# Performance work log

Measured on AMD Instinct MI355X. Metric: run time of the kernel, lower is better.

## Reference

```python
import math
import jax, jax.numpy as jnp
import numpy as np

L, B, D = 2048, 8, 1024
Z, H, N = 128, 2048, 16


def setup_inputs() -> dict:
    key = jax.random.key(0)
    ks = jax.random.split(key, 16)
    s = 0.02
    inp = {
        "x": jax.random.normal(ks[0], (L, B, D), jnp.float32),
        "ln_w": jnp.ones((D,), jnp.float32),
        "ln_b": jnp.zeros((D,), jnp.float32),
        "v_w": jax.random.normal(ks[1], (H, D), jnp.float32) * s,
        "v_b": jnp.zeros((H,), jnp.float32),
        "mx_w": jax.random.normal(ks[2], (Z + H + 2 * D, D), jnp.float32) * s,
        "mx_b": jnp.zeros((Z + H + 2 * D,), jnp.float32),
        "h_w": jax.random.normal(ks[3], (D, H), jnp.float32) * s,
        "h_b": jnp.zeros((D,), jnp.float32),
        "qk_gamma": jnp.ones((2, Z), jnp.float32) + jax.random.normal(ks[4], (2, Z), jnp.float32) * s,
        "qk_beta": jax.random.normal(ks[5], (2, Z), jnp.float32) * s,
        "ema_delta": jax.random.normal(ks[6], (D, N, 1), jnp.float32),
        "ema_alpha": jax.random.normal(ks[7], (D, N, 1), jnp.float32),
        "ema_beta": jax.random.normal(ks[8], (D, N, 1), jnp.float32) * s,
        "ema_gamma": jax.random.normal(ks[9], (D, N), jnp.float32) * s,
        "ema_omega": jax.random.normal(ks[10], (D,), jnp.float32) * s,
        "rb_alpha": jax.random.normal(ks[11], (1, Z), jnp.float32) * s,
        "rb_beta": jax.random.normal(ks[12], (1, Z), jnp.float32) * s,
    }
    return inp


def _rotary_bias(rb_alpha, rb_beta, seq_len, z):
    # RotaryRelativePositionalBias.forward(seq_len) -> (L, L)
    half = z // 2
    freqs = jnp.exp(jnp.arange(half, dtype=jnp.float32) * (-math.log(10000.0) / half))
    pos = jnp.arange(seq_len, dtype=jnp.float32)[:, None] * freqs[None, :]  # (L, half)
    sin, cos = jnp.sin(pos), jnp.cos(pos)

    def rot(w):  # (1, Z) -> (L, Z)
        we = jnp.broadcast_to(w, (seq_len, z))
        w1, w2 = we[:, :half], we[:, half:]
        return jnp.concatenate([w1 * cos - w2 * sin, w2 * cos + w1 * sin], axis=1)

    return rot(rb_alpha) @ rot(rb_beta).T  # (L, L)


def _ema(xn, ema_delta, ema_alpha, ema_beta, ema_gamma, ema_omega):
    # xn: (L, B, D) -> damped multi-head EMA via FFT causal conv (MEGA MultiHeadEMA)
    seq_len = xn.shape[0]
    p = jax.nn.sigmoid(ema_delta)           # (D, N, 1)
    a = jax.nn.sigmoid(ema_alpha)           # (D, N, 1)
    q = 1.0 - p * a                         # (D, N, 1)
    t = jnp.arange(seq_len, dtype=jnp.float32)[None, None, :]
    kern = (p * ema_beta) * jnp.exp(t * jnp.log(q))          # (D, N, L)
    scale = math.sqrt(1.0 / kern.shape[1])
    k_dl = jnp.einsum("dnl,dn->dl", kern, ema_gamma * scale)  # (D, L)
    xt = jnp.transpose(xn, (1, 2, 0))        # (B, D, L)
    nfft = 2 * seq_len
    kf = jnp.fft.rfft(k_dl, n=nfft)          # (D, F)
    xf = jnp.fft.rfft(xt, n=nfft)            # (B, D, F)
    conv = jnp.fft.irfft(xf * kf, n=nfft)[..., :seq_len]      # (B, D, L)
    return jax.nn.silu(jnp.transpose(conv, (2, 0, 1)) + xn * ema_omega)  # (L, B, D)


def reference(x, ln_w, ln_b, v_w, v_b, mx_w, mx_b, h_w, h_b, qk_gamma, qk_beta,
              ema_delta, ema_alpha, ema_beta, ema_gamma, ema_omega, rb_alpha, rb_beta):
    seq_len, bsz, d = x.shape
    residual = x
    # prenorm LayerNorm
    mu = jnp.mean(x, axis=-1, keepdims=True)
    var = jnp.mean(jnp.square(x - mu), axis=-1, keepdims=True)
    xn = (x - mu) * jax.lax.rsqrt(var + 1e-5) * ln_w + ln_b

    v = jax.nn.silu(xn @ v_w.T + v_b)                          # (L, B, H)
    mx = _ema(xn, ema_delta, ema_alpha, ema_beta, ema_gamma, ema_omega)
    base = mx @ mx_w.T + mx_b                                  # (L, B, Z+H+2D)
    u = jax.nn.sigmoid(base[..., :d])                          # update gate
    zr = jax.nn.silu(base[..., d:d + Z + H])
    hx = base[..., d + Z + H:]
    z, r = zr[..., :Z], zr[..., Z:]                            # (L,B,Z), (L,B,H)
    z2 = z[:, :, None, :] * qk_gamma + qk_beta                 # (L, B, 2, Z)
    q = jnp.transpose(z2[:, :, 0], (1, 0, 2)) * (Z ** -0.5)    # (B, L, Z)
    k = jnp.transpose(z2[:, :, 1], (1, 0, 2))                  # (B, L, Z)
    vb = jnp.transpose(v, (1, 0, 2))                           # (B, L, H)

    bias = _rotary_bias(rb_alpha, rb_beta, seq_len, Z)         # (L, L)
    attn = jax.nn.softmax(jnp.einsum("blz,bmz->blm", q, k) + bias, axis=-1)
    h = jnp.transpose(jnp.einsum("blm,bmh->blh", attn, vb), (1, 0, 2))  # (L, B, H)
    h = jax.nn.silu(hx + (h * r) @ h_w.T + h_b)                # (L, B, D)
    return residual + u * (h - residual)
```

## Files before the change

kernel.cpp:

```cpp
#include <hip/hip_runtime.h>
#include <cstdint>
#include <cstddef>

typedef __bf16 bf16;
typedef __bf16 bf16x8 __attribute__((ext_vector_type(8)));
typedef float  f32x4  __attribute__((ext_vector_type(4)));

#define DEVI static __device__ __forceinline__

DEVI float fsigmoid(float x) { return 1.0f / (1.0f + __expf(-x)); }
DEVI float fsilu(float x)    { return x / (1.0f + __expf(-x)); }

DEVI unsigned short b16bits(float v) { bf16 h = (bf16)v; return __builtin_bit_cast(unsigned short, h); }
DEVI float lo16f(unsigned int w) { return __builtin_bit_cast(float, w << 16); }
DEVI float hi16f(unsigned int w) { return __builtin_bit_cast(float, w & 0xffff0000u); }

DEVI float waveRedSum(float v) {
#pragma unroll
  for (int o = 32; o > 0; o >>= 1) v += __shfl_xor(v, o, 64);
  return v;
}
DEVI float waveRedMax(float v) {
#pragma unroll
  for (int o = 32; o > 0; o >>= 1) v = fmaxf(v, __shfl_xor(v, o, 64));
  return v;
}

DEVI void xcd_swizzle(int& bx, int& by) {
  const int gx = gridDim.x, gy = gridDim.y;
  const int nwg = gx * gy;
  const int flat = blockIdx.y * gx + blockIdx.x;
  const int xcd = flat & 7;
  const int rem = nwg & 7;
  const int q = nwg >> 3;
  const int base = (xcd < rem) ? xcd * (q + 1) : rem * (q + 1) + (xcd - rem) * q;
  const int swz = base + (flat >> 3);
  bx = swz % gx;
  by = swz / gx;
}

struct alignas(8) B4 { bf16 x, y, z, w; };

__global__ __launch_bounds__(256) void k_copyout(const float* __restrict__ x, float* __restrict__ o)
{
  const long i = (long)blockIdx.x * 256 + threadIdx.x;
  ((float4*)o)[i] = ((const float4*)x)[i];
}

__global__ __launch_bounds__(256) void k_lnstats(const float* __restrict__ x, float* __restrict__ stats)
{
  const long t = blockIdx.x;
  const int tid = threadIdx.x;
  const float4 v = ((const float4*)(x + t * 1024))[tid];
  float s  = v.x + v.y + v.z + v.w;
  float s2 = v.x * v.x + v.y * v.y + v.z * v.z + v.w * v.w;
  __shared__ float red[2][4];
  s = waveRedSum(s);
  s2 = waveRedSum(s2);
  const int wv = tid >> 6, ln = tid & 63;
  if (ln == 0) { red[0][wv] = s; red[1][wv] = s2; }
  __syncthreads();
  if (tid == 0) {
    s  = red[0][0] + red[0][1] + red[0][2] + red[0][3];
    s2 = red[1][0] + red[1][1] + red[1][2] + red[1][3];
    const float mu  = s * (1.0f / 1024.0f);
    const float var = s2 * (1.0f / 1024.0f) - mu * mu;
    stats[2 * t]     = mu;
    stats[2 * t + 1] = rsqrtf(var + 1e-5f);
  }
}

__global__ __launch_bounds__(256) void k_cvt(const float* __restrict__ in, bf16* __restrict__ out, int n4)
{
  const int i = blockIdx.x * 256 + threadIdx.x;
  if (i >= n4) return;
  const float4 v = ((const float4*)in)[i];
  B4 h; h.x = (bf16)v.x; h.y = (bf16)v.y; h.z = (bf16)v.z; h.w = (bf16)v.w;
  ((B4*)out)[i] = h;
}

__global__ __launch_bounds__(256) void k_ema_coeff(
    const float* __restrict__ de, const float* __restrict__ al,
    const float* __restrict__ be, const float* __restrict__ ga,
    float* __restrict__ qv, float* __restrict__ cv)
{
  const int i = blockIdx.x * 256 + threadIdx.x;
  const int d = i >> 4, n = i & 15;
  const float p = 1.0f / (1.0f + expf(-de[i]));
  const float a = 1.0f / (1.0f + expf(-al[i]));
  qv[n * 1024 + d] = 1.0f - p * a;
  cv[n * 1024 + d] = p * be[i] * ga[i] * 0.25f;
}

__global__ __launch_bounds__(256) void k_ema(
    const float* __restrict__ x, const float* __restrict__ stats,
    const float* __restrict__ lnw, const float* __restrict__ lnb,
    const float* __restrict__ qv, const float* __restrict__ cv,
    const float* __restrict__ omega, bf16* __restrict__ mx)
{
  const int d = blockIdx.x * 256 + threadIdx.x;
  const int b = blockIdx.y;
  float q[16], c[16], s[16];
#pragma unroll
  for (int n = 0; n < 16; ++n) {
    q[n] = qv[n * 1024 + d];
    c[n] = cv[n * 1024 + d];
    s[n] = 0.0f;
  }
  const float om = omega[d], wd = lnw[d], bd = lnb[d];
  const float* xp = x + (long)b * 1024 + d;
  bf16* mp = mx + (long)b * 1024 + d;
  float buf[8], nxt[8];
  float2 bst[8], nst[8];
#pragma unroll
  for (int i = 0; i < 8; ++i) {
    buf[i] = xp[(long)i * 8192];
    bst[i] = ((const float2*)stats)[(long)i * 8 + b];
  }
  for (int l0 = 0; l0 < 2048; l0 += 8) {
    if (l0 + 8 < 2048) {
#pragma unroll
      for (int i = 0; i < 8; ++i) {
        nxt[i] = xp[(long)(l0 + 8 + i) * 8192];
        nst[i] = ((const float2*)stats)[(long)(l0 + 8 + i) * 8 + b];
      }
    }
#pragma unroll
    for (int i = 0; i < 8; ++i) {
      const float xv = (buf[i] - bst[i].x) * bst[i].y * wd + bd;
      float p0 = 0.f, p1 = 0.f, p2 = 0.f, p3 = 0.f;
#pragma unroll
      for (int n = 0; n < 16; n += 4) {
        s[n]     = fmaf(q[n],     s[n],     xv);
        s[n + 1] = fmaf(q[n + 1], s[n + 1], xv);
        s[n + 2] = fmaf(q[n + 2], s[n + 2], xv);
        s[n + 3] = fmaf(q[n + 3], s[n + 3], xv);
        p0 = fmaf(c[n],     s[n],     p0);
        p1 = fmaf(c[n + 1], s[n + 1], p1);
        p2 = fmaf(c[n + 2], s[n + 2], p2);
        p3 = fmaf(c[n + 3], s[n + 3], p3);
      }
      const float pre = fmaf(xv, om, (p0 + p1) + (p2 + p3));
      mp[(long)(l0 + i) * 8192] = (bf16)fsilu(pre);
    }
#pragma unroll
    for (int i = 0; i < 8; ++i) { buf[i] = nxt[i]; bst[i] = nst[i]; }
  }
}

__global__ __launch_bounds__(64) void k_rotfill(
    const float* __restrict__ rba, const float* __restrict__ rbb,
    bf16* __restrict__ Qp, bf16* __restrict__ Kp)
{
  const int l = blockIdx.x, zi = threadIdx.x;
  const float fr = __expf(-0.14391156831212787f * (float)zi);
  const float pos = (float)l * fr;
  const float sn = sinf(pos), cs = cosf(pos);
  const float a1 = rba[zi], a2 = rba[64 + zi];
  const float b1 = rbb[zi], b2 = rbb[64 + zi];
  const bf16 qa = (bf16)(a1 * cs - a2 * sn);
  const bf16 qb = (bf16)(a2 * cs + a1 * sn);
  const bf16 ka = (bf16)(b1 * cs - b2 * sn);
  const bf16 kb = (bf16)(b2 * cs + b1 * sn);
#pragma unroll
  for (int b = 0; b < 8; ++b) {
    const long base = ((long)b * 2048 + l) * 256;
    Qp[base + 128 + zi] = qa;
    Qp[base + 192 + zi] = qb;
    Kp[base + 128 + zi] = ka;
    Kp[base + 192 + zi] = kb;
  }
}

__global__ __launch_bounds__(256) void k_softmax(float* __restrict__ S)
{
  const long row = blockIdx.x;
  float* sp = S + row * 2048;
  const int tid = threadIdx.x;
  float vals[8];
  float mx = -1e30f;
#pragma unroll
  for (int i = 0; i < 8; ++i) { vals[i] = sp[i * 256 + tid]; mx = fmaxf(mx, vals[i]); }
  __shared__ float red[4];
  mx = waveRedMax(mx);
  const int wv = tid >> 6, ln = tid & 63;
  if (ln == 0) red[wv] = mx;
  __syncthreads();
  mx = fmaxf(fmaxf(red[0], red[1]), fmaxf(red[2], red[3]));
  float sum = 0.f;
#pragma unroll
  for (int i = 0; i < 8; ++i) { vals[i] = __expf(vals[i] - mx); sum += vals[i]; }
  __syncthreads();
  sum = waveRedSum(sum);
  if (ln == 0) red[wv] = sum;
  __syncthreads();
  sum = red[0] + red[1] + red[2] + red[3];
  const float inv = 1.0f / sum;
  bf16* pp = (bf16*)sp;
#pragma unroll
  for (int i = 0; i < 8; ++i) pp[i * 256 + tid] = (bf16)(vals[i] * inv);
}

__global__ __launch_bounds__(1024) void k_vtrans8(
    const bf16* __restrict__ v, bf16* __restrict__ vt, const int eoff)
{
  __shared__ bf16 tile[32][33];
  const int l0 = blockIdx.x * 32, h0 = blockIdx.y * 32, b = blockIdx.z;
  const int tx = threadIdx.x, ty = threadIdx.y;
  tile[ty][tx] = v[((long)(l0 + ty) * 8 + b) * 256 + h0 + tx];
  __syncthreads();
  vt[((long)b * 2048 + eoff + h0 + ty) * 2048 + l0 + tx] = tile[tx][ty];
}

DEVI void gload16(const void* g, void* l) {
  __builtin_amdgcn_global_load_lds(
      (__attribute__((address_space(1))) void*)(void*)g,
      (__attribute__((address_space(3))) void*)l, 16, 0, 0);
}

template<int EPI>
__global__ __launch_bounds__(256) void k_gemm_bt(
    const bf16* __restrict__ A, const bf16* __restrict__ Bm,
    const int K, const int lda, const int ldb,
    const float* __restrict__ bias,
    void* __restrict__ o0, void* __restrict__ o1, void* __restrict__ o2, void* __restrict__ o3,
    const void* __restrict__ e0, const void* __restrict__ e1, const void* __restrict__ e2)
{
  __shared__ alignas(16) bf16 As[128 * 64];
  __shared__ alignas(16) bf16 Bs[128 * 64];
  const int tid = threadIdx.x;
  const int wave = tid >> 6, lane = tid & 63;
  const int wm = wave >> 1, wn = wave & 1;
  int bx, by;
  xcd_swizzle(bx, by);
  const int tm = by * 128, tn = bx * 128;
  const int fr = lane & 15, kg = lane >> 4;

  f32x4 acc[4][4];
  const f32x4 z4 = {0.0f, 0.0f, 0.0f, 0.0f};
#pragma unroll
  for (int i = 0; i < 4; ++i)
#pragma unroll
    for (int j = 0; j < 4; ++j) acc[i][j] = z4;

  const int est = wave * 512 + lane * 8;
  const int srow = est >> 6;
  const int scol = est & 63;
  const long arow = (long)(tm + srow);
  const long brow = (long)(tn + srow);

  for (int k0 = 0; k0 < K; k0 += 64) {
    __syncthreads();
#pragma unroll
    for (int cc = 0; cc < 4; ++cc) {
      gload16(A + (arow + cc * 32) * lda + k0 + scol, As + cc * 2048 + wave * 512);
      gload16(Bm + (brow + cc * 32) * ldb + k0 + scol, Bs + cc * 2048 + wave * 512);
    }
    __syncthreads();
    bf16x8 af[2][4], bfv[2][4];
#pragma unroll
    for (int ks = 0; ks < 2; ++ks)
#pragma unroll
      for (int i = 0; i < 4; ++i) {
        af[ks][i]  = *(const bf16x8*)&As[(wm * 64 + i * 16 + fr) * 64 + ks * 32 + kg * 8];
        bfv[ks][i] = *(const bf16x8*)&Bs[(wn * 64 + i * 16 + fr) * 64 + ks * 32 + kg * 8];
      }
#pragma unroll
    for (int ks = 0; ks < 2; ++ks)
#pragma unroll
      for (int i = 0; i < 4; ++i)
#pragma unroll
        for (int j = 0; j < 4; ++j)
          acc[i][j] = __builtin_amdgcn_mfma_f32_16x16x32_bf16(af[ks][i], bfv[ks][j], acc[i][j], 0, 0, 0);
  }

#pragma unroll
  for (int i = 0; i < 4; ++i) {
#pragma unroll
    for (int j = 0; j < 4; ++j) {
#pragma unroll
      for (int rr = 0; rr < 4; ++rr) {
        const int row = tm + wm * 64 + i * 16 + kg * 4 + rr;
        const int col = tn + wn * 64 + j * 16 + fr;
        const float a = acc[i][j][rr];
        if constexpr (EPI == 1) {
          const float tv = a + bias[col];
          if (col < 1024) {
            ((unsigned short*)o0)[((long)row * 1024 + col) * 2] = b16bits(fsigmoid(tv));
          } else if (col < 1152) {
            const int zi = col - 1024;
            const float zval = fsilu(tv);
            const float qq = (zval * ((const float*)e0)[zi] + ((const float*)e1)[zi]) * 0.08838834764831845f;
            const float kk =  zval * ((const float*)e0)[128 + zi] + ((const float*)e1)[128 + zi];
            const long base = ((long)(row & 7) * 2048 + (row >> 3)) * 256 + zi;
            ((bf16*)o2)[base] = (bf16)qq;
            ((bf16*)o3)[base] = (bf16)kk;
          } else if (col < 3200) {
            ((bf16*)o1)[(long)row * 2048 + (col - 1152)] = (bf16)fsilu(tv);
          } else {
            ((unsigned short*)o0)[((long)row * 1024 + (col - 3200)) * 2 + 1] = b16bits(tv);
          }
        } else if constexpr (EPI == 2) {
          ((float*)o0)[(long)row * 2048 + col] = a;
        } else if constexpr (EPI == 3) {
          const long idx = (long)row * 16384 + col;
          const float rv = (float)((const bf16*)e0)[idx];
          ((bf16*)o0)[idx] = (bf16)(a * rv);
        } else if constexpr (EPI == 4) {
          const long idx = (long)row * 1024 + col;
          const unsigned int w = ((const unsigned int*)o0)[idx];
          const float uv = lo16f(w), hxv = hi16f(w);
          const float hval = fsilu(hxv + a + bias[col]);
          const float xv = ((const float*)e1)[idx];
          ((float*)o0)[idx] = xv + uv * (hval - xv);
        }
      }
    }
  }
}

__global__ __launch_bounds__(256) void k_gemm_lnA(
    const float* __restrict__ x, const float* __restrict__ stats,
    const float* __restrict__ lnw, const float* __restrict__ lnb,
    const bf16* __restrict__ Bm, const float* __restrict__ bias,
    bf16* __restrict__ out)
{
  __shared__ alignas(16) bf16 As[128 * 64];
  __shared__ alignas(16) bf16 Bs[128 * 64];
  __shared__ float smu[128], srs[128];
  const int tid = threadIdx.x;
  const int wave = tid >> 6, lane = tid & 63;
  const int wm = wave >> 1, wn = wave & 1;
  int bx, by;
  xcd_swizzle(bx, by);
  const int tm = by * 128, tn = bx * 128;
  const int fr = lane & 15, kg = lane >> 4;
  if (tid < 128) {
    smu[tid] = stats[2 * (long)(tm + tid)];
    srs[tid] = stats[2 * (long)(tm + tid) + 1];
  }

  f32x4 acc[4][4];
  const f32x4 z4 = {0.0f, 0.0f, 0.0f, 0.0f};
#pragma unroll
  for (int i = 0; i < 4; ++i)
#pragma unroll
    for (int j = 0; j < 4; ++j) acc[i][j] = z4;

  const int est = wave * 512 + lane * 8;
  const int srow = est >> 6, scol = est & 63;
  const long brow = (long)(tn + srow);
  const int ar = tid & 127, ah = (tid >> 7) * 32;
  const float* xrow = x + (long)(tm + ar) * 1024 + ah;

  for (int k0 = 0; k0 < 1024; k0 += 64) {
    __syncthreads();
#pragma unroll
    for (int cc = 0; cc < 4; ++cc)
      gload16(Bm + (brow + cc * 32) * 1024 + k0 + scol, Bs + cc * 2048 + wave * 512);
    {
      const float mu = smu[ar], rs = srs[ar];
      bf16 tmp[32];
#pragma unroll
      for (int i = 0; i < 8; ++i) {
        const float4 xv = ((const float4*)(xrow + k0))[i];
        const float4 wv = ((const float4*)(lnw + k0 + ah))[i];
        const float4 bv = ((const float4*)(lnb + k0 + ah))[i];
        tmp[i * 4 + 0] = (bf16)((xv.x - mu) * rs * wv.x + bv.x);
        tmp[i * 4 + 1] = (bf16)((xv.y - mu) * rs * wv.y + bv.y);
        tmp[i * 4 + 2] = (bf16)((xv.z - mu) * rs * wv.z + bv.z);
        tmp[i * 4 + 3] = (bf16)((xv.w - mu) * rs * wv.w + bv.w);
      }
      const int sw = (ar & 7) << 3;
#pragma unroll
      for (int i = 0; i < 4; ++i)
        *(bf16x8*)&As[ar * 64 + ((ah + i * 8) ^ sw)] = *(const bf16x8*)&tmp[i * 8];
    }
    __syncthreads();
    bf16x8 af[2][4], bfv[2][4];
#pragma unroll
    for (int ks = 0; ks < 2; ++ks)
#pragma unroll
      for (int i = 0; i < 4; ++i) {
        const int ar2 = wm * 64 + i * 16 + fr;
        af[ks][i]  = *(const bf16x8*)&As[ar2 * 64 + ((ks * 32 + kg * 8) ^ ((ar2 & 7) << 3))];
        bfv[ks][i] = *(const bf16x8*)&Bs[(wn * 64 + i * 16 + fr) * 64 + ks * 32 + kg * 8];
      }
#pragma unroll
    for (int ks = 0; ks < 2; ++ks)
#pragma unroll
      for (int i = 0; i < 4; ++i)
#pragma unroll
        for (int j = 0; j < 4; ++j)
          acc[i][j] = __builtin_amdgcn_mfma_f32_16x16x32_bf16(af[ks][i], bfv[ks][j], acc[i][j], 0, 0, 0);
  }

#pragma unroll
  for (int i = 0; i < 4; ++i)
#pragma unroll
    for (int j = 0; j < 4; ++j)
#pragma unroll
      for (int rr = 0; rr < 4; ++rr) {
        const int row = tm + wm * 64 + i * 16 + kg * 4 + rr;
        const int col = tn + wn * 64 + j * 16 + fr;
        out[(long)row * 256 + col] = (bf16)fsilu(acc[i][j][rr] + bias[col]);
      }
}

extern "C" void kernel_launch(void* const* d_in, const int* in_sizes, int n_in,
                              void* d_out, int out_size, void* d_ws, size_t ws_size,
                              hipStream_t stream)
{
  const float* x    = (const float*)d_in[0];
  const float* ln_w = (const float*)d_in[1];
  const float* ln_b = (const float*)d_in[2];
  const float* v_w  = (const float*)d_in[3];
  const float* v_b  = (const float*)d_in[4];
  const float* mx_w = (const float*)d_in[5];
  const float* mx_b = (const float*)d_in[6];
  const float* h_w  = (const float*)d_in[7];
  const float* h_b  = (const float*)d_in[8];
  const float* qk_g = (const float*)d_in[9];
  const float* qk_b = (const float*)d_in[10];
  const float* e_de = (const float*)d_in[11];
  const float* e_al = (const float*)d_in[12];
  const float* e_be = (const float*)d_in[13];
  const float* e_ga = (const float*)d_in[14];
  const float* e_om = (const float*)d_in[15];
  const float* rb_a = (const float*)d_in[16];
  const float* rb_b = (const float*)d_in[17];

  const size_t MiB = 1048576UL;
  if (ws_size < 160 * MiB) {
    k_copyout<<<16384, 256, 0, stream>>>(x, (float*)d_out);
    return;
  }

  char* ws = (char*)d_ws;
  bf16*  rbuf  = (bf16*)(ws + 0 * MiB);
  bf16*  v_t   = (bf16*)(ws + 64 * MiB);
  bf16*  mxw_h = (bf16*)(ws + 64 * MiB);
  bf16*  mxb   = (bf16*)(ws + 73 * MiB);
  float* qv    = (float*)(ws + 105 * MiB);
  float* cv    = (float*)(ws + 105 * MiB + 65536);
  bf16*  Qp    = (bf16*)(ws + 128 * MiB);
  bf16*  hw_h  = (bf16*)(ws + 128 * MiB);
  bf16*  Kp    = (bf16*)(ws + 136 * MiB);
  float* Sbuf  = (float*)(ws + 144 * MiB);
  bf16*  vw_h  = (bf16*)(ws + 144 * MiB);
  bf16*  vbufe = (bf16*)(ws + 148 * MiB);
  float* stats = (float*)(ws + 156 * MiB);

  k_lnstats<<<16384, 256, 0, stream>>>(x, stats);
  k_cvt<<<2048, 256, 0, stream>>>(v_w, vw_h, 524288);
  k_cvt<<<4224, 256, 0, stream>>>(mx_w, mxw_h, 1081344);
  k_ema_coeff<<<64, 256, 0, stream>>>(e_de, e_al, e_be, e_ga, qv, cv);
  k_ema<<<dim3(4, 8), 256, 0, stream>>>(x, stats, ln_w, ln_b, qv, cv, e_om, mxb);

  k_gemm_bt<1><<<dim3(33, 128, 1), 256, 0, stream>>>(mxb, mxw_h, 1024, 1024, 1024,
      mx_b, d_out, (void*)rbuf, (void*)Qp, (void*)Kp, (const void*)qk_g, (const void*)qk_b, nullptr);
  k_rotfill<<<2048, 64, 0, stream>>>(rb_a, rb_b, Qp, Kp);

  for (int e = 0; e < 8; ++e) {
    k_gemm_lnA<<<dim3(2, 128, 1), 256, 0, stream>>>(x, stats, ln_w, ln_b,
        vw_h + (long)e * 256 * 1024, v_b + e * 256, vbufe);
    k_vtrans8<<<dim3(64, 8, 8), dim3(32, 32), 0, stream>>>(vbufe, v_t, e * 256);
  }

  for (int b = 0; b < 8; ++b) {
    const bf16* Ab = Qp + (long)b * 524288;
    const bf16* Bb = Kp + (long)b * 524288;
    k_gemm_bt<2><<<dim3(16, 16, 1), 256, 0, stream>>>(Ab, Bb, 256, 256, 256,
        nullptr, (void*)Sbuf, nullptr, nullptr, nullptr, nullptr, nullptr, nullptr);
    k_softmax<<<2048, 256, 0, stream>>>(Sbuf);
    bf16* hrp = rbuf + (long)b * 2048;
    k_gemm_bt<3><<<dim3(16, 16, 1), 256, 0, stream>>>((const bf16*)Sbuf, v_t + (long)b * 4194304,
        2048, 4096, 2048, nullptr, (void*)hrp, nullptr, nullptr, nullptr, (const void*)hrp, nullptr, nullptr);
  }

  k_cvt<<<2048, 256, 0, stream>>>(h_w, hw_h, 524288);

  k_gemm_bt<4><<<dim3(8, 128, 1), 256, 0, stream>>>(rbuf, hw_h, 2048, 2048, 2048,
      h_b, d_out, nullptr, nullptr, nullptr, nullptr, (const void*)x, nullptr);
}
```

Before: 1.791 ms.

## Parallelize EMA recurrence with a chunked three-pass scan; split gate GEMM launch

After: 1.596 ms, median of 4. -10.9%, faster.

```diff
diff --git a/kernel.cpp b/kernel.cpp
--- a/kernel.cpp
+++ b/kernel.cpp
@@ -92,42 +92,89 @@
   cv[n * 1024 + d] = p * be[i] * ga[i] * 0.25f;
 }
 
-__global__ __launch_bounds__(256) void k_ema(
+__global__ __launch_bounds__(256) void k_ema_scan1(
+    const float* __restrict__ x, const float* __restrict__ stats,
+    const float* __restrict__ lnw, const float* __restrict__ lnb,
+    const float* __restrict__ qv, float* __restrict__ scan)
+{
+  const int d = blockIdx.x * 256 + threadIdx.x;
+  const int b = blockIdx.y, c = blockIdx.z;
+  float q[16], s[16];
+#pragma unroll
+  for (int n = 0; n < 16; ++n) { q[n] = qv[n * 1024 + d]; s[n] = 0.0f; }
+  const float wd = lnw[d], bd = lnb[d];
+  const float* xp = x + (long)b * 1024 + d;
+  const int l0 = c * 128;
+  for (int j0 = 0; j0 < 128; j0 += 8) {
+    float xr[8]; float2 st[8];
+#pragma unroll
+    for (int i = 0; i < 8; ++i) {
+      const int l = l0 + j0 + i;
+      xr[i] = xp[(long)l * 8192];
+      st[i] = ((const float2*)stats)[(long)l * 8 + b];
+    }
+#pragma unroll
+    for (int i = 0; i < 8; ++i) {
+      const float xv = (xr[i] - st[i].x) * st[i].y * wd + bd;
+#pragma unroll
+      for (int n = 0; n < 16; ++n) s[n] = fmaf(q[n], s[n], xv);
+    }
+  }
+  float* sp = scan + ((((long)c * 8 + b) * 1024) + d) * 16;
+#pragma unroll
+  for (int n = 0; n < 16; ++n) sp[n] = s[n];
+}
+
+__global__ __launch_bounds__(256) void k_ema_scan2(
+    const float* __restrict__ qv, float* __restrict__ scan)
+{
+  const int i = blockIdx.x * 256 + threadIdx.x;
+  const int n = i & 15, d = (i >> 4) & 1023, b = i >> 14;
+  const float q = qv[n * 1024 + d];
+  const float q2 = q * q, q4 = q2 * q2, q8 = q4 * q4;
+  const float q16 = q8 * q8, q32 = q16 * q16, q64 = q32 * q32, q128 = q64 * q64;
+  float carry = 0.0f;
+#pragma unroll
+  for (int c = 0; c < 16; ++c) {
+    const long off = ((((long)c * 8 + b) * 1024) + d) * 16 + n;
+    const float t = scan[off];
+    scan[off] = carry;
+    carry = fmaf(q128, carry, t);
+  }
+}
+
+__global__ __launch_bounds__(256) void k_ema_apply(
     const float* __restrict__ x, const float* __restrict__ stats,
     const float* __restrict__ lnw, const float* __restrict__ lnb,
     const float* __restrict__ qv, const float* __restrict__ cv,
-    const float* __restrict__ omega, bf16* __restrict__ mx)
+    const float* __restrict__ omega, const float* __restrict__ scan,
+    bf16* __restrict__ mx)
 {
   const int d = blockIdx.x * 256 + threadIdx.x;
-  const int b = blockIdx.y;
-  float q[16], c[16], s[16];
+  const int b = blockIdx.y, c = blockIdx.z;
+  float q[16], cc[16], s[16];
+  const float* sp = scan + ((((long)c * 8 + b) * 1024) + d) * 16;
 #pragma unroll
   for (int n = 0; n < 16; ++n) {
     q[n] = qv[n * 1024 + d];
-    c[n] = cv[n * 1024 + d];
-    s[n] = 0.0f;
+    cc[n] = cv[n * 1024 + d];
+    s[n] = sp[n];
   }
   const float om = omega[d], wd = lnw[d], bd = lnb[d];
   const float* xp = x + (long)b * 1024 + d;
   bf16* mp = mx + (long)b * 1024 + d;
-  float buf[8], nxt[8];
-  float2 bst[8], nst[8];
-#pragma unroll
-  for (int i = 0; i < 8; ++i) {
-    buf[i] = xp[(long)i * 8192];
-    bst[i] = ((const float2*)stats)[(long)i * 8 + b];
-  }
-  for (int l0 = 0; l0 < 2048; l0 += 8) {
-    if (l0 + 8 < 2048) {
-#pragma unroll
-      for (int i = 0; i < 8; ++i) {
-        nxt[i] = xp[(long)(l0 + 8 + i) * 8192];
-        nst[i] = ((const float2*)stats)[(long)(l0 + 8 + i) * 8 + b];
-      }
-    }
+  const int l0 = c * 128;
+  for (int j0 = 0; j0 < 128; j0 += 8) {
+    float xr[8]; float2 st[8];
 #pragma unroll
     for (int i = 0; i < 8; ++i) {
-      const float xv = (buf[i] - bst[i].x) * bst[i].y * wd + bd;
+      const int l = l0 + j0 + i;
+      xr[i] = xp[(long)l * 8192];
+      st[i] = ((const float2*)stats)[(long)l * 8 + b];
+    }
+#pragma unroll
+    for (int i = 0; i < 8; ++i) {
+      const float xv = (xr[i] - st[i].x) * st[i].y * wd + bd;
       float p0 = 0.f, p1 = 0.f, p2 = 0.f, p3 = 0.f;
 #pragma unroll
       for (int n = 0; n < 16; n += 4) {
@@ -135,16 +182,14 @@
         s[n + 1] = fmaf(q[n + 1], s[n + 1], xv);
         s[n + 2] = fmaf(q[n + 2], s[n + 2], xv);
         s[n + 3] = fmaf(q[n + 3], s[n + 3], xv);
-        p0 = fmaf(c[n],     s[n],     p0);
-        p1 = fmaf(c[n + 1], s[n + 1], p1);
-        p2 = fmaf(c[n + 2], s[n + 2], p2);
-        p3 = fmaf(c[n + 3], s[n + 3], p3);
+        p0 = fmaf(cc[n],     s[n],     p0);
+        p1 = fmaf(cc[n + 1], s[n + 1], p1);
+        p2 = fmaf(cc[n + 2], s[n + 2], p2);
+        p3 = fmaf(cc[n + 3], s[n + 3], p3);
       }
       const float pre = fmaf(xv, om, (p0 + p1) + (p2 + p3));
-      mp[(long)(l0 + i) * 8192] = (bf16)fsilu(pre);
-    }
-#pragma unroll
-    for (int i = 0; i < 8; ++i) { buf[i] = nxt[i]; bst[i] = nst[i]; }
+      mp[(long)(l0 + j0 + i) * 8192] = (bf16)fsilu(pre);
+    }
   }
 }
 
@@ -221,7 +266,7 @@
 template<int EPI>
 __global__ __launch_bounds__(256) void k_gemm_bt(
     const bf16* __restrict__ A, const bf16* __restrict__ Bm,
-    const int K, const int lda, const int ldb,
+    const int K, const int lda, const int ldb, const int coladd,
     const float* __restrict__ bias,
     void* __restrict__ o0, void* __restrict__ o1, void* __restrict__ o2, void* __restrict__ o3,
     const void* __restrict__ e0, const void* __restrict__ e1, const void* __restrict__ e2)
@@ -281,7 +326,7 @@
 #pragma unroll
       for (int rr = 0; rr < 4; ++rr) {
         const int row = tm + wm * 64 + i * 16 + kg * 4 + rr;
-        const int col = tn + wn * 64 + j * 16 + fr;
+        const int col = coladd + tn + wn * 64 + j * 16 + fr;
         const float a = acc[i][j][rr];
         if constexpr (EPI == 1) {
           const float tv = a + bias[col];
@@ -448,6 +493,7 @@
   bf16*  Kp    = (bf16*)(ws + 136 * MiB);
   float* Sbuf  = (float*)(ws + 144 * MiB);
   bf16*  vw_h  = (bf16*)(ws + 144 * MiB);
+  float* scanb = (float*)(ws + 148 * MiB);
   bf16*  vbufe = (bf16*)(ws + 148 * MiB);
   float* stats = (float*)(ws + 156 * MiB);
 
@@ -455,10 +501,16 @@
   k_cvt<<<2048, 256, 0, stream>>>(v_w, vw_h, 524288);
   k_cvt<<<4224, 256, 0, stream>>>(mx_w, mxw_h, 1081344);
   k_ema_coeff<<<64, 256, 0, stream>>>(e_de, e_al, e_be, e_ga, qv, cv);
-  k_ema<<<dim3(4, 8), 256, 0, stream>>>(x, stats, ln_w, ln_b, qv, cv, e_om, mxb);
-
-  k_gemm_bt<1><<<dim3(33, 128, 1), 256, 0, stream>>>(mxb, mxw_h, 1024, 1024, 1024,
-      mx_b, d_out, (void*)rbuf, (void*)Qp, (void*)Kp, (const void*)qk_g, (const void*)qk_b, nullptr);
+
+  k_ema_scan1<<<dim3(4, 8, 16), 256, 0, stream>>>(x, stats, ln_w, ln_b, qv, scanb);
+  k_ema_scan2<<<512, 256, 0, stream>>>(qv, scanb);
+  k_ema_apply<<<dim3(4, 8, 16), 256, 0, stream>>>(x, stats, ln_w, ln_b, qv, cv, e_om, scanb, mxb);
+
+  for (int sp = 0; sp < 3; ++sp) {
+    k_gemm_bt<1><<<dim3(11, 128, 1), 256, 0, stream>>>(mxb, mxw_h + (long)sp * 1408 * 1024,
+        1024, 1024, 1024, sp * 1408,
+        mx_b, d_out, (void*)rbuf, (void*)Qp, (void*)Kp, (const void*)qk_g, (const void*)qk_b, nullptr);
+  }
   k_rotfill<<<2048, 64, 0, stream>>>(rb_a, rb_b, Qp, Kp);
 
   for (int e = 0; e < 8; ++e) {
@@ -470,16 +522,16 @@
   for (int b = 0; b < 8; ++b) {
     const bf16* Ab = Qp + (long)b * 524288;
     const bf16* Bb = Kp + (long)b * 524288;
-    k_gemm_bt<2><<<dim3(16, 16, 1), 256, 0, stream>>>(Ab, Bb, 256, 256, 256,
+    k_gemm_bt<2><<<dim3(16, 16, 1), 256, 0, stream>>>(Ab, Bb, 256, 256, 256, 0,
         nullptr, (void*)Sbuf, nullptr, nullptr, nullptr, nullptr, nullptr, nullptr);
     k_softmax<<<2048, 256, 0, stream>>>(Sbuf);
     bf16* hrp = rbuf + (long)b * 2048;
     k_gemm_bt<3><<<dim3(16, 16, 1), 256, 0, stream>>>((const bf16*)Sbuf, v_t + (long)b * 4194304,
-        2048, 4096, 2048, nullptr, (void*)hrp, nullptr, nullptr, nullptr, (const void*)hrp, nullptr, nullptr);
+        2048, 4096, 2048, 0, nullptr, (void*)hrp, nullptr, nullptr, nullptr, (const void*)hrp, nullptr, nullptr);
   }
 
   k_cvt<<<2048, 256, 0, stream>>>(h_w, hw_h, 524288);
 
-  k_gemm_bt<4><<<dim3(8, 128, 1), 256, 0, stream>>>(rbuf, hw_h, 2048, 2048, 2048,
+  k_gemm_bt<4><<<dim3(8, 128, 1), 256, 0, stream>>>(rbuf, hw_h, 2048, 2048, 2048, 0,
       h_b, d_out, nullptr, nullptr, nullptr, nullptr, (const void*)x, nullptr);
 }
```
